# Kernel tuning notes

Measured on AMD Instinct MI355X. Metric: run time of the kernel, lower is better.

The kernel has to match this reference:

```python
import jax, jax.numpy as jnp
import numpy as np

BETA = 0.25


def setup_inputs() -> dict:
    key = jax.random.key(0)
    k1, k2, k3 = jax.random.split(key, 3)
    B, T, D, K = 4, 2048, 512, 16384
    z_e = jax.random.normal(k1, (B, T, D), dtype=jnp.float32)
    codebook = jax.random.normal(k2, (K, D), dtype=jnp.float32)  # frozen embedding
    # nn.Linear(D, D, bias=False) weight, scaled like kaiming-uniform magnitude
    W = jax.random.normal(k3, (D, D), dtype=jnp.float32) * (1.0 / np.sqrt(D))
    return {"z_e": z_e, "codebook": codebook, "W": W}


def reference(z_e, codebook, W):
    B, T, D = z_e.shape
    # effective codebook: Linear(codebook) = codebook @ W.T   -> (K, D)
    eff = jnp.matmul(codebook, W.T)
    z_flat = z_e.reshape(-1, D)  # (N, D)
    # squared euclidean distances (argmin-equivalent to cdist p=2)
    d2 = (
        jnp.sum(z_flat * z_flat, axis=1, keepdims=True)  # (N,1)
        - 2.0 * jnp.matmul(z_flat, eff.T)                  # (N,K)
        + jnp.sum(eff * eff, axis=1)[None, :]              # (1,K)
    )
    code_indices = jnp.argmin(d2, axis=1)  # (N,)
    z_q = eff[code_indices].reshape(B, T, D)
    loss_w = jnp.mean((jax.lax.stop_gradient(z_e) - z_q) ** 2)
    loss_commit = BETA * jnp.mean((z_e - jax.lax.stop_gradient(z_q)) ** 2)
    total_loss = loss_w + loss_commit
    # straight-through estimator
    z_q_out = z_e + jax.lax.stop_gradient(z_q - z_e)
    return z_q_out, total_loss, code_indices.reshape(B, T)
```

## Files before the change

### kernel.cpp

```cpp
#include <hip/hip_runtime.h>
#include <stdint.h>


#define N_ROWS 8192
#define DIM    512
#define K_CB   16384
#define TILE_F16 16384
#define HALF_F16 8192
#define KT_EFF 24
#define KT_D   8
#define TILE_P8 16384
#define HALF_P8 8192
#define PAN_P8  ((size_t)KT_D * TILE_P8)
#define RMARGIN 28.0f

typedef _Float16 f16x8 __attribute__((ext_vector_type(8)));
typedef float f32x4 __attribute__((ext_vector_type(4)));
typedef long lx2 __attribute__((ext_vector_type(2)));

#define FENCE() asm volatile("" ::: "memory")
#define BARRIER() do { FENCE(); __builtin_amdgcn_s_barrier(); FENCE(); } while (0)
#define VMCNT(n) asm volatile("s_waitcnt vmcnt(" #n ")" ::: "memory")

__device__ __forceinline__ void gload_lds16(const void* g, void* l) {
  __builtin_amdgcn_global_load_lds(
      (const __attribute__((address_space(1))) uint32_t*)g,
      (__attribute__((address_space(3))) uint32_t*)l, 16, 0, 0);
}

__device__ __forceinline__ unsigned cvt2_fp8(float a, float b) {
  unsigned r;
  asm("v_cvt_pk_fp8_f32 %0, %1, %2" : "=v"(r) : "v"(a), "v"(b));
  return r & 0xFFFFu;
}

__global__ __launch_bounds__(256) void split_tiled_kernel(
    const float* __restrict__ S, _Float16* __restrict__ T, int resid_limb) {
  const int b = blockIdx.x;
  const int mp = b / 48;
  const int r1 = b % 48;
  const int kt = r1 >> 1, half = r1 & 1;
  const int limb = kt >> 3;
  const int ksrc = (kt & 7) * 64;
  const bool resid = (limb == resid_limb);
  const int t = threadIdx.x;
  _Float16* dst = T + ((size_t)(mp * KT_EFF + kt) * 2 + half) * HALF_F16;
#pragma unroll
  for (int cc = 0; cc < 4; ++cc) {
    const int ci = cc * 256 + t;
    const int kblk = ci >> 7, row = ci & 127;
    const int m = mp * 256 + half * 128 + row;
    const float* src = &S[(size_t)m * DIM + ksrc + kblk * 8];
    float4 x0 = *reinterpret_cast<const float4*>(src);
    float4 x1 = *reinterpret_cast<const float4*>(src + 4);
    const float xs[8] = {x0.x, x0.y, x0.z, x0.w, x1.x, x1.y, x1.z, x1.w};
    f16x8 o;
    if (!resid) {
#pragma unroll
      for (int j = 0; j < 8; ++j) o[j] = (_Float16)xs[j];
    } else {
#pragma unroll
      for (int j = 0; j < 8; ++j) {
        _Float16 h = (_Float16)xs[j];
        o[j] = (_Float16)(xs[j] - (float)h);
      }
    }
    *reinterpret_cast<f16x8*>(&dst[(size_t)ci * 8]) = o;
  }
}

__global__ __launch_bounds__(256) void split1_kernel(
    const float* __restrict__ S, uint8_t* __restrict__ T) {
  const int b = blockIdx.x;
  const int p = b >> 4;
  const int r1 = b & 15;
  const int kt = r1 >> 1, half = r1 & 1;
  const int ksrc = kt * 64;
  const int t = threadIdx.x;
  uint8_t* dst = T + ((size_t)(p * KT_D + kt) * 2 + half) * HALF_P8;
#pragma unroll
  for (int cc = 0; cc < 4; ++cc) {
    const int ci = cc * 256 + t;
    const int kblk = ci >> 7, row = ci & 127;
    const int m = p * 256 + half * 128 + row;
    const float* src = &S[(size_t)m * DIM + ksrc + kblk * 8];
    float4 x0 = *reinterpret_cast<const float4*>(src);
    float4 x1 = *reinterpret_cast<const float4*>(src + 4);
    const unsigned lo = cvt2_fp8(x0.x, x0.y) | (cvt2_fp8(x0.z, x0.w) << 16);
    const unsigned hi = cvt2_fp8(x1.x, x1.y) | (cvt2_fp8(x1.z, x1.w) << 16);
    const uint64_t pack = (uint64_t)lo | ((uint64_t)hi << 32);
    const int q = kblk & 3, h2 = kblk >> 2;
    *reinterpret_cast<uint64_t*>(&dst[(size_t)(q * 128 + row) * 16 + h2 * 8]) =
        pack;
  }
}

__global__ __launch_bounds__(256) void effgemm128_kernel(
    const _Float16* __restrict__ CpT, const _Float16* __restrict__ WpT,
    float* __restrict__ eff, uint8_t* __restrict__ BpT) {
  __shared__ __align__(16) _Float16 lbuf[2][2][HALF_F16];
  const int tid = threadIdx.x;
  const int w = tid >> 6, lane = tid & 63;
  const int lh = lane & 15, lq = lane >> 4;
  const int wr = w >> 1, wc = w & 1;
  const int bid = blockIdx.x;
  const int nb = bid & 3, mh = bid >> 2;
  const int pA = mh >> 1, hA = mh & 1;
  const int pB = nb >> 1, hB = nb & 1;
  f32x4 acc[4][4] = {};

  auto stage = [&](int kt, int buf) {
    const _Float16* a = CpT + (((size_t)pA * KT_EFF + kt) * 2 + hA) * HALF_F16;
    const _Float16* b = WpT + (((size_t)pB * KT_EFF + kt) * 2 + hB) * HALF_F16;
#pragma unroll
    for (int i = 0; i < 4; ++i) {
      const int off = i * 2048 + w * 512;
      gload_lds16(a + off + lane * 8, &lbuf[buf][0][off]);
      gload_lds16(b + off + lane * 8, &lbuf[buf][1][off]);
    }
  };

  stage(0, 0);
  for (int kt = 0; kt < KT_EFF; ++kt) {
    __syncthreads();
    if (kt + 1 < KT_EFF) stage(kt + 1, (kt + 1) & 1);
    const _Float16* At = &lbuf[kt & 1][0][0];
    const _Float16* Bt = &lbuf[kt & 1][1][0];
    f16x8 af[4][2], bf[4][2];
#pragma unroll
    for (int mf = 0; mf < 4; ++mf) {
      const int r = wr * 64 + mf * 16 + lh;
#pragma unroll
      for (int kk = 0; kk < 2; ++kk)
        af[mf][kk] = *reinterpret_cast<const f16x8*>(
            &At[((kk * 4 + lq) * 128 + r) * 8]);
    }
#pragma unroll
    for (int nf = 0; nf < 4; ++nf) {
      const int r = wc * 64 + nf * 16 + lh;
#pragma unroll
      for (int kk = 0; kk < 2; ++kk)
        bf[nf][kk] = *reinterpret_cast<const f16x8*>(
            &Bt[((kk * 4 + lq) * 128 + r) * 8]);
    }
    __builtin_amdgcn_s_setprio(1);
#pragma unroll
    for (int kk = 0; kk < 2; ++kk)
#pragma unroll
      for (int mf = 0; mf < 4; ++mf)
#pragma unroll
        for (int nf = 0; nf < 4; ++nf)
          acc[mf][nf] = __builtin_amdgcn_mfma_f32_16x16x32_f16(
              af[mf][kk], bf[nf][kk], acc[mf][nf], 0, 0, 0);
    __builtin_amdgcn_s_setprio(0);
  }

#pragma unroll
  for (int mf = 0; mf < 4; ++mf)
#pragma unroll
    for (int nf = 0; nf < 4; ++nf) {
      const int cl = wc * 64 + nf * 16 + lh;
      const int col = nb * 128 + cl;
      const int ktd = col >> 6, kd = col & 63;
      const int q = (kd >> 3) & 3, h2 = kd >> 5, jb = kd & 7;
      const unsigned c01 = cvt2_fp8(acc[mf][nf][0], acc[mf][nf][1]);
      const unsigned c23 = cvt2_fp8(acc[mf][nf][2], acc[mf][nf][3]);
#pragma unroll
      for (int j = 0; j < 4; ++j) {
        const int rl = wr * 64 + mf * 16 + lq * 4 + j;
        const int row = mh * 128 + rl;
        eff[(size_t)row * DIM + col] = acc[mf][nf][j];
        const unsigned byte =
            (j < 2 ? (c01 >> (j * 8)) : (c23 >> ((j - 2) * 8))) & 255u;
        BpT[((((size_t)(row >> 8) * KT_D + ktd) * 2 + ((row >> 7) & 1)) * 4 + q)
                * 2048 + (row & 127) * 16 + h2 * 8 + jb] = (uint8_t)byte;
      }
    }
}

__global__ __launch_bounds__(256) void effnorm_kernel(
    const float* __restrict__ E, float* __restrict__ En) {
  const int w = threadIdx.x >> 6;
  const int lane = threadIdx.x & 63;
  const int row = blockIdx.x * 4 + w;
  const float* er = &E[(size_t)row * DIM];
  float s = 0.f;
#pragma unroll
  for (int k = 0; k < DIM / 64; ++k) {
    float v = er[lane + k * 64];
    s = fmaf(v, v, s);
  }
#pragma unroll
  for (int o = 32; o; o >>= 1) s += __shfl_down(s, o, 64);
  if (lane == 0) En[row] = s;
}


__device__ __forceinline__ void stage_half8(const uint8_t* src, uint8_t* ldsb,
                                            int tid) {
  gload_lds16(src + tid * 16, ldsb + tid * 16);
}

template <int MQ>
__device__ __forceinline__ void read_a8(const uint8_t* At, int wr, int lh, int lq,
                                        lx2 af[4]) {
#pragma unroll
  for (int m2 = 0; m2 < 4; ++m2) {
    const int row = wr * 128 + (MQ * 4 + m2) * 16 + lh;
    const int half = row >> 7, r = row & 127;
    af[m2] = *reinterpret_cast<const lx2*>(
        &At[(size_t)half * 8192 + (lq * 128 + r) * 16]);
  }
}

template <int NQ>
__device__ __forceinline__ void read_b8(const uint8_t* Bt, int wc, int lh, int lq,
                                        lx2 bf[4]) {
#pragma unroll
  for (int n2 = 0; n2 < 2; ++n2) {
    const int row = wc * 64 + (NQ * 2 + n2) * 16 + lh;
    const int half = row >> 7, r = row & 127;
    bf[NQ * 2 + n2] = *reinterpret_cast<const lx2*>(
        &Bt[(size_t)half * 8192 + (lq * 128 + r) * 16]);
  }
}

template <int MQ, int NQ>
__device__ __forceinline__ void mfma_phase8(const lx2 af[4], const lx2 bf[4],
                                            f32x4 acc[8][4]) {
  __builtin_amdgcn_s_setprio(1);
#pragma unroll
  for (int kk = 0; kk < 2; ++kk)
#pragma unroll
    for (int m2 = 0; m2 < 4; ++m2)
#pragma unroll
      for (int n2 = 0; n2 < 2; ++n2)
        acc[MQ * 4 + m2][NQ * 2 + n2] = __builtin_amdgcn_mfma_f32_16x16x32_fp8_fp8(
            af[m2][kk], bf[NQ * 2 + n2][kk], acc[MQ * 4 + m2][NQ * 2 + n2], 0, 0, 0);
  __builtin_amdgcn_s_setprio(0);
}

__device__ __forceinline__ void pipeline8_p8(
    const uint8_t* Ab, const uint8_t* Bb, uint8_t (&lds)[4][TILE_P8],
    f32x4 (&acc)[8][4], int tid, int wr, int wc, int lh, int lq, int NT) {
  lx2 af[4], bf[4];
  stage_half8(Ab, &lds[0][0], tid);
  stage_half8(Ab + HALF_P8, &lds[0][HALF_P8], tid);
  stage_half8(Bb, &lds[1][0], tid);
  stage_half8(Bb + HALF_P8, &lds[1][HALF_P8], tid);
  stage_half8(Bb + TILE_P8, &lds[3][0], tid);
  stage_half8(Bb + TILE_P8 + HALF_P8, &lds[3][HALF_P8], tid);
  stage_half8(Ab + TILE_P8, &lds[2][0], tid);
  VMCNT(3);
  BARRIER();
  for (int t = 0; t < NT; ++t) {
    const int s = t & 1;
    const uint8_t* At = &lds[s * 2 + 0][0];
    const uint8_t* Bt = &lds[s * 2 + 1][0];
    read_a8<0>(At, wr, lh, lq, af);
    read_b8<0>(Bt, wc, lh, lq, bf);
    if (t + 1 < NT)
      stage_half8(Ab + (size_t)(t + 1) * TILE_P8 + HALF_P8,
                  &lds[(s ^ 1) * 2][HALF_P8], tid);
    BARRIER();
    mfma_phase8<0, 0>(af, bf, acc);
    BARRIER();
    read_b8<1>(Bt, wc, lh, lq, bf);
    BARRIER();
    mfma_phase8<0, 1>(af, bf, acc);
    BARRIER();
    read_a8<1>(At, wr, lh, lq, af);
    if (t + 2 < NT)
      stage_half8(Bb + (size_t)(t + 2) * TILE_P8, &lds[s * 2 + 1][0], tid);
    BARRIER();
    mfma_phase8<1, 1>(af, bf, acc);
    BARRIER();
    if (t + 2 < NT) {
      stage_half8(Bb + (size_t)(t + 2) * TILE_P8 + HALF_P8,
                  &lds[s * 2 + 1][HALF_P8], tid);
      stage_half8(Ab + (size_t)(t + 2) * TILE_P8, &lds[s * 2][0], tid);
    }
    BARRIER();
    mfma_phase8<1, 0>(af, bf, acc);
    if (t == NT - 2) { VMCNT(0); } else { VMCNT(3); }
    BARRIER();
  }
}

__global__ __launch_bounds__(512) void dist1_kernel(
    const uint8_t* __restrict__ ApT, const uint8_t* __restrict__ BpT,
    const float* __restrict__ En, float* __restrict__ gv,
    unsigned* __restrict__ gmask) {
  __shared__ __align__(16) uint8_t lds[4][TILE_P8];
  const int tid = threadIdx.x;
  const int w = tid >> 6, lane = tid & 63;
  const int lh = lane & 15, lq = lane >> 4;
  const int wr = w >> 2, wc = w & 3;
  const int bid = blockIdx.x;
  const int xcd = bid & 7, c = bid >> 3;
  const int np = xcd * 8 + (c & 7);
  const int mp = c >> 3;
  f32x4 acc[8][4] = {};
  pipeline8_p8(ApT + (size_t)mp * PAN_P8, BpT + (size_t)np * PAN_P8, lds, acc,
               tid, wr, wc, lh, lq, KT_D);
  float en[4];
#pragma unroll
  for (int nf = 0; nf < 4; ++nf)
    en[nf] = En[np * 256 + wc * 64 + nf * 16 + lh];
#pragma unroll
  for (int mf = 0; mf < 8; ++mf) {
#pragma unroll
    for (int j = 0; j < 4; ++j) {
      const float s0 = fmaf(-2.f, acc[mf][0][j], en[0]);
      const float s1 = fmaf(-2.f, acc[mf][1][j], en[1]);
      const float s2 = fmaf(-2.f, acc[mf][2][j], en[2]);
      const float s3 = fmaf(-2.f, acc[mf][3][j], en[3]);
      float v0 = fminf(s0, s1);
      float v1 = fminf(s2, s3);
#pragma unroll
      for (int m = 1; m < 16; m <<= 1) {
        v0 = fminf(v0, __shfl_xor(v0, m, 64));
        v1 = fminf(v1, __shfl_xor(v1, m, 64));
      }
      const unsigned long long b0 = __ballot(s0 <= v0 + RMARGIN);
      const unsigned long long b1 = __ballot(s1 <= v0 + RMARGIN);
      const unsigned long long b2 = __ballot(s2 <= v1 + RMARGIN);
      const unsigned long long b3 = __ballot(s3 <= v1 + RMARGIN);
      if (lh == 0) {
        const int row = mp * 256 + wr * 128 + mf * 16 + lq * 4 + j;
        const unsigned w0 = (unsigned)((b0 >> (lq * 16)) & 0xFFFFull) |
                            ((unsigned)((b1 >> (lq * 16)) & 0xFFFFull) << 16);
        const unsigned w1 = (unsigned)((b2 >> (lq * 16)) & 0xFFFFull) |
                            ((unsigned)((b3 >> (lq * 16)) & 0xFFFFull) << 16);
        float2* gp = (float2*)&gv[(size_t)row * 512 + np * 8 + wc * 2];
        *gp = make_float2(v0, v1);
        uint2* mq = (uint2*)&gmask[(size_t)row * 512 + np * 8 + wc * 2];
        *mq = make_uint2(w0, w1);
      }
    }
  }
}

__global__ __launch_bounds__(256) void refine_kernel(
    const float* __restrict__ Z, const float* __restrict__ E,
    const float* __restrict__ En, const float* __restrict__ gv,
    const unsigned* __restrict__ gmask, float* __restrict__ zq,
    float* __restrict__ out_idx, float* __restrict__ ploss) {
  const int row = blockIdx.x * 4 + (threadIdx.x >> 6);
  const int lane = threadIdx.x & 63;
  const int hl = lane & 31;
  const int hi = lane >> 5;

  float v[8];
#pragma unroll
  for (int i = 0; i < 8; ++i) v[i] = gv[(size_t)row * 512 + i * 64 + lane];
  float A = fminf(fminf(fminf(v[0], v[1]), fminf(v[2], v[3])),
                  fminf(fminf(v[4], v[5]), fminf(v[6], v[7])));
#pragma unroll
  for (int m = 1; m < 64; m <<= 1) A = fminf(A, __shfl_xor(A, m, 64));
  const float thr = A + RMARGIN;

  float4 zr0, zr1, zr2, zr3;
  {
    const float4* zp = (const float4*)(Z + (size_t)row * 512 + hl * 16);
    zr0 = zp[0]; zr1 = zp[1]; zr2 = zp[2]; zr3 = zp[3];
  }

  float bv = 3.0e38f;
  int bi = 2147483647;
#pragma unroll 1
  for (int i = 0; i < 8; ++i) {
    unsigned long long bm = __ballot(v[i] <= thr);
    while (bm) {
      const int l = __builtin_ctzll(bm);
      bm &= bm - 1;
      const int g = i * 64 + l;
      unsigned m = gmask[(size_t)row * 512 + g];
      while (m) {
        const int c0 = __builtin_ctz(m);
        m &= m - 1;
        int c1 = -1;
        if (m) { c1 = __builtin_ctz(m); m &= m - 1; }
        const int cl = hi ? c1 : c0;
        const bool act = (cl >= 0);
        const int col = g * 32 + (act ? cl : c0);
        const float4* er = (const float4*)(E + (size_t)col * 512 + hl * 16);
        const float4 e0 = er[0], e1 = er[1], e2 = er[2], e3 = er[3];
        float p = 0.f;
        p = fmaf(zr0.x, e0.x, p); p = fmaf(zr0.y, e0.y, p);
        p = fmaf(zr0.z, e0.z, p); p = fmaf(zr0.w, e0.w, p);
        p = fmaf(zr1.x, e1.x, p); p = fmaf(zr1.y, e1.y, p);
        p = fmaf(zr1.z, e1.z, p); p = fmaf(zr1.w, e1.w, p);
        p = fmaf(zr2.x, e2.x, p); p = fmaf(zr2.y, e2.y, p);
        p = fmaf(zr2.z, e2.z, p); p = fmaf(zr2.w, e2.w, p);
        p = fmaf(zr3.x, e3.x, p); p = fmaf(zr3.y, e3.y, p);
        p = fmaf(zr3.z, e3.z, p); p = fmaf(zr3.w, e3.w, p);
#pragma unroll
        for (int s2 = 1; s2 < 32; s2 <<= 1) p += __shfl_xor(p, s2, 64);
        const float vv = fmaf(-2.f, p, En[col]);
        if (act && (vv < bv || (vv == bv && col < bi))) { bv = vv; bi = col; }
      }
    }
  }
#pragma unroll
  for (int s2 = 1; s2 < 64; s2 <<= 1) {
    const float v2 = __shfl_xor(bv, s2, 64);
    const int i2 = __shfl_xor(bi, s2, 64);
    if (v2 < bv || (v2 == bv && i2 < bi)) { bv = v2; bi = i2; }
  }
  const int idx = bi;

  const float4* e4 = (const float4*)(E + (size_t)idx * 512 + lane * 8);
  const float4* z4 = (const float4*)(Z + (size_t)row * 512 + lane * 8);
  float4* q4 = (float4*)(zq + (size_t)row * 512 + lane * 8);
  const float4 ea = e4[0], eb = e4[1];
  const float4 za = z4[0], zb = z4[1];
  q4[0] = ea; q4[1] = eb;
  float s = 0.f;
  s = fmaf(za.x - ea.x, za.x - ea.x, s); s = fmaf(za.y - ea.y, za.y - ea.y, s);
  s = fmaf(za.z - ea.z, za.z - ea.z, s); s = fmaf(za.w - ea.w, za.w - ea.w, s);
  s = fmaf(zb.x - eb.x, zb.x - eb.x, s); s = fmaf(zb.y - eb.y, zb.y - eb.y, s);
  s = fmaf(zb.z - eb.z, zb.z - eb.z, s); s = fmaf(zb.w - eb.w, zb.w - eb.w, s);
#pragma unroll
  for (int o = 32; o; o >>= 1) s += __shfl_down(s, o, 64);
  if (lane == 0) {
    ploss[row] = s;
    out_idx[row] = (float)idx;
  }
}

__global__ __launch_bounds__(256) void loss_final_kernel(
    const float* __restrict__ ploss, float* __restrict__ out_loss) {
  const int t = threadIdx.x;
  double s = 0.0;
  for (int i = t; i < N_ROWS; i += 256) s += (double)ploss[i];
#pragma unroll
  for (int o = 32; o; o >>= 1) s += __shfl_down(s, o, 64);
  __shared__ double ds[4];
  if ((t & 63) == 0) ds[t >> 6] = s;
  __syncthreads();
  if (t == 0) {
    double tot = ds[0] + ds[1] + ds[2] + ds[3];
    out_loss[0] = (float)(1.25 * tot / ((double)N_ROWS * (double)DIM));
  }
}


extern "C" void kernel_launch(void* const* d_in, const int* in_sizes, int n_in,
                              void* d_out, int out_size, void* d_ws, size_t ws_size,
                              hipStream_t stream) {
  const float* z_e      = (const float*)d_in[0];
  const float* codebook = (const float*)d_in[1];
  const float* W        = (const float*)d_in[2];
  float* out = (float*)d_out;
  char* ws = (char*)d_ws;

  float*          eff     = (float*)(ws);
  float*          effnorm = (float*)(ws + 33554432);
  _Float16*       WpT     = (_Float16*)(ws + 33619968);
  float*          ploss   = (float*)(ws + 36274176);
  _Float16*       CpT     = (_Float16*)(ws + 36306944);
  float*          gv      = (float*)(ws + 36306944);
  uint8_t*        ApT     = (uint8_t*)(ws + 53084160);
  unsigned*       gmask   = (unsigned*)(ws + 61472768);
  uint8_t*        BpT     = (uint8_t*)(ws + 86638592);

  float* out_zq   = out;
  float* out_loss = out + (size_t)N_ROWS * DIM;
  float* out_idx  = out + (size_t)N_ROWS * DIM + 1;

  split_tiled_kernel<<<64 * 48, 256, 0, stream>>>(codebook, CpT, 2);
  split_tiled_kernel<<<2 * 48, 256, 0, stream>>>(W, WpT, 1);
  effgemm128_kernel<<<512, 256, 0, stream>>>(CpT, WpT, eff, BpT);
  effnorm_kernel<<<K_CB / 4, 256, 0, stream>>>(eff, effnorm);
  split1_kernel<<<32 * 16, 256, 0, stream>>>(z_e, ApT);
  dist1_kernel<<<2048, 512, 0, stream>>>(ApT, BpT, effnorm, gv, gmask);
  refine_kernel<<<N_ROWS / 4, 256, 0, stream>>>(z_e, eff, effnorm, gv, gmask,
                                                out_zq, out_idx, ploss);
  loss_final_kernel<<<1, 256, 0, stream>>>(ploss, out_loss);
}
```

Baseline: 295.6 us.

## Add fp16 intermediate screening stage in refine before exact fp32 rescoring

Adds a kernel that converts the effective codebook to fp16. The refine kernel now scores the fp8-screened candidates with fp16 codebook rows, which halves the gather bytes per candidate, and stores the scores in shared memory. Only candidates within a small margin of the fp16 minimum are then rescored exactly in fp32 over the full wavefront. This cuts fp32 gather traffic in refine, at the cost of an extra conversion pass over the 32 MB codebook, a third screening stage, and a risk of mis-selection if the fp16 error exceeds the 0.5 margin.

Result: slower. 302.8 us (+2.4%).

```diff
diff --git a/kernel.cpp b/kernel.cpp
--- a/kernel.cpp
+++ b/kernel.cpp
@@ -13,6 +13,8 @@
 #define HALF_P8 8192
 #define PAN_P8  ((size_t)KT_D * TILE_P8)
 #define RMARGIN 28.0f
+#define TMARG   0.5f
+#define MAXC    256
 
 typedef _Float16 f16x8 __attribute__((ext_vector_type(8)));
 typedef float f32x4 __attribute__((ext_vector_type(4)));
@@ -176,6 +178,24 @@
                 * 2048 + (row & 127) * 16 + h2 * 8 + jb] = (uint8_t)byte;
       }
     }
+}
+
+__global__ __launch_bounds__(256) void eff16_kernel(
+    const float* __restrict__ E, _Float16* __restrict__ E16) {
+  const size_t base = ((size_t)blockIdx.x * 256 + threadIdx.x) * 16;
+  const float4* s = (const float4*)(E + base);
+  const float4 a = s[0], b = s[1], c = s[2], d = s[3];
+  f16x8 lo, hi;
+  lo[0] = (_Float16)a.x; lo[1] = (_Float16)a.y;
+  lo[2] = (_Float16)a.z; lo[3] = (_Float16)a.w;
+  lo[4] = (_Float16)b.x; lo[5] = (_Float16)b.y;
+  lo[6] = (_Float16)b.z; lo[7] = (_Float16)b.w;
+  hi[0] = (_Float16)c.x; hi[1] = (_Float16)c.y;
+  hi[2] = (_Float16)c.z; hi[3] = (_Float16)c.w;
+  hi[4] = (_Float16)d.x; hi[5] = (_Float16)d.y;
+  hi[6] = (_Float16)d.z; hi[7] = (_Float16)d.w;
+  *reinterpret_cast<f16x8*>(E16 + base) = lo;
+  *reinterpret_cast<f16x8*>(E16 + base + 8) = hi;
 }
 
 __global__ __launch_bounds__(256) void effnorm_kernel(
@@ -343,13 +363,17 @@
 
 __global__ __launch_bounds__(256) void refine_kernel(
     const float* __restrict__ Z, const float* __restrict__ E,
-    const float* __restrict__ En, const float* __restrict__ gv,
-    const unsigned* __restrict__ gmask, float* __restrict__ zq,
-    float* __restrict__ out_idx, float* __restrict__ ploss) {
-  const int row = blockIdx.x * 4 + (threadIdx.x >> 6);
+    const _Float16* __restrict__ E16, const float* __restrict__ En,
+    const float* __restrict__ gv, const unsigned* __restrict__ gmask,
+    float* __restrict__ zq, float* __restrict__ out_idx,
+    float* __restrict__ ploss) {
+  const int w = threadIdx.x >> 6;
+  const int row = blockIdx.x * 4 + w;
   const int lane = threadIdx.x & 63;
   const int hl = lane & 31;
   const int hi = lane >> 5;
+  __shared__ float ss[4][MAXC];
+  __shared__ int sc[4][MAXC];
 
   float v[8];
 #pragma unroll
@@ -365,9 +389,27 @@
     const float4* zp = (const float4*)(Z + (size_t)row * 512 + hl * 16);
     zr0 = zp[0]; zr1 = zp[1]; zr2 = zp[2]; zr3 = zp[3];
   }
+  const float4* z4 = (const float4*)(Z + (size_t)row * 512 + lane * 8);
+  const float4 za = z4[0], zb = z4[1];
 
   float bv = 3.0e38f;
   int bi = 2147483647;
+
+  auto exact64 = [&](int colu) {
+    const float4* er = (const float4*)(E + (size_t)colu * 512 + lane * 8);
+    const float4 ea4 = er[0], eb4 = er[1];
+    float p = 0.f;
+    p = fmaf(za.x, ea4.x, p); p = fmaf(za.y, ea4.y, p);
+    p = fmaf(za.z, ea4.z, p); p = fmaf(za.w, ea4.w, p);
+    p = fmaf(zb.x, eb4.x, p); p = fmaf(zb.y, eb4.y, p);
+    p = fmaf(zb.z, eb4.z, p); p = fmaf(zb.w, eb4.w, p);
+#pragma unroll
+    for (int s2 = 1; s2 < 64; s2 <<= 1) p += __shfl_xor(p, s2, 64);
+    const float vv = fmaf(-2.f, p, En[colu]);
+    if (vv < bv || (vv == bv && colu < bi)) { bv = vv; bi = colu; }
+  };
+
+  int nc = 0;
 #pragma unroll 1
   for (int i = 0; i < 8; ++i) {
     unsigned long long bm = __ballot(v[i] <= thr);
@@ -381,40 +423,53 @@
         m &= m - 1;
         int c1 = -1;
         if (m) { c1 = __builtin_ctz(m); m &= m - 1; }
+        const bool act = (c1 >= 0);
         const int cl = hi ? c1 : c0;
-        const bool act = (cl >= 0);
-        const int col = g * 32 + (act ? cl : c0);
-        const float4* er = (const float4*)(E + (size_t)col * 512 + hl * 16);
-        const float4 e0 = er[0], e1 = er[1], e2 = er[2], e3 = er[3];
-        float p = 0.f;
-        p = fmaf(zr0.x, e0.x, p); p = fmaf(zr0.y, e0.y, p);
-        p = fmaf(zr0.z, e0.z, p); p = fmaf(zr0.w, e0.w, p);
-        p = fmaf(zr1.x, e1.x, p); p = fmaf(zr1.y, e1.y, p);
-        p = fmaf(zr1.z, e1.z, p); p = fmaf(zr1.w, e1.w, p);
-        p = fmaf(zr2.x, e2.x, p); p = fmaf(zr2.y, e2.y, p);
-        p = fmaf(zr2.z, e2.z, p); p = fmaf(zr2.w, e2.w, p);
-        p = fmaf(zr3.x, e3.x, p); p = fmaf(zr3.y, e3.y, p);
-        p = fmaf(zr3.z, e3.z, p); p = fmaf(zr3.w, e3.w, p);
-#pragma unroll
-        for (int s2 = 1; s2 < 32; s2 <<= 1) p += __shfl_xor(p, s2, 64);
-        const float vv = fmaf(-2.f, p, En[col]);
-        if (act && (vv < bv || (vv == bv && col < bi))) { bv = vv; bi = col; }
+        const int col = g * 32 + ((hi && act) ? c1 : c0);
+        (void)cl;
+        if (nc < MAXC - 1) {
+          const f16x8 ea = *reinterpret_cast<const f16x8*>(
+              E16 + (size_t)col * 512 + hl * 16);
+          const f16x8 eb = *reinterpret_cast<const f16x8*>(
+              E16 + (size_t)col * 512 + hl * 16 + 8);
+          float p = 0.f;
+          p = fmaf((float)ea[0], zr0.x, p); p = fmaf((float)ea[1], zr0.y, p);
+          p = fmaf((float)ea[2], zr0.z, p); p = fmaf((float)ea[3], zr0.w, p);
+          p = fmaf((float)ea[4], zr1.x, p); p = fmaf((float)ea[5], zr1.y, p);
+          p = fmaf((float)ea[6], zr1.z, p); p = fmaf((float)ea[7], zr1.w, p);
+          p = fmaf((float)eb[0], zr2.x, p); p = fmaf((float)eb[1], zr2.y, p);
+          p = fmaf((float)eb[2], zr2.z, p); p = fmaf((float)eb[3], zr2.w, p);
+          p = fmaf((float)eb[4], zr3.x, p); p = fmaf((float)eb[5], zr3.y, p);
+          p = fmaf((float)eb[6], zr3.z, p); p = fmaf((float)eb[7], zr3.w, p);
+#pragma unroll
+          for (int s2 = 1; s2 < 32; s2 <<= 1) p += __shfl_xor(p, s2, 64);
+          const float vv = fmaf(-2.f, p, En[col]);
+          if (lane == 0) { ss[w][nc] = vv; sc[w][nc] = col; }
+          if (lane == 32 && act) { ss[w][nc + 1] = vv; sc[w][nc + 1] = col; }
+          nc += act ? 2 : 1;
+        } else {
+          exact64(g * 32 + c0);
+          if (act) exact64(g * 32 + c1);
+        }
       }
     }
   }
-#pragma unroll
-  for (int s2 = 1; s2 < 64; s2 <<= 1) {
-    const float v2 = __shfl_xor(bv, s2, 64);
-    const int i2 = __shfl_xor(bi, s2, 64);
-    if (v2 < bv || (v2 == bv && i2 < bi)) { bv = v2; bi = i2; }
+
+  float m16 = 3.0e38f;
+  for (int q = lane; q < nc; q += 64) m16 = fminf(m16, ss[w][q]);
+#pragma unroll
+  for (int s2 = 1; s2 < 64; s2 <<= 1) m16 = fminf(m16, __shfl_xor(m16, s2, 64));
+  const float thr2 = m16 + TMARG;
+#pragma unroll 1
+  for (int q = 0; q < nc; ++q) {
+    const float sv = ss[w][q];
+    if (sv <= thr2) exact64(sc[w][q]);
   }
   const int idx = bi;
 
   const float4* e4 = (const float4*)(E + (size_t)idx * 512 + lane * 8);
-  const float4* z4 = (const float4*)(Z + (size_t)row * 512 + lane * 8);
   float4* q4 = (float4*)(zq + (size_t)row * 512 + lane * 8);
   const float4 ea = e4[0], eb = e4[1];
-  const float4 za = z4[0], zb = z4[1];
   q4[0] = ea; q4[1] = eb;
   float s = 0.f;
   s = fmaf(za.x - ea.x, za.x - ea.x, s); s = fmaf(za.y - ea.y, za.y - ea.y, s);
@@ -461,9 +516,10 @@
   float*          ploss   = (float*)(ws + 36274176);
   _Float16*       CpT     = (_Float16*)(ws + 36306944);
   float*          gv      = (float*)(ws + 36306944);
-  uint8_t*        ApT     = (uint8_t*)(ws + 53084160);
-  unsigned*       gmask   = (unsigned*)(ws + 61472768);
+  unsigned*       gmask   = (unsigned*)(ws + 53084160);
+  _Float16*       eff16   = (_Float16*)(ws + 69861376);
   uint8_t*        BpT     = (uint8_t*)(ws + 86638592);
+  uint8_t*        ApT     = (uint8_t*)(ws + 95027200);
 
   float* out_zq   = out;
   float* out_loss = out + (size_t)N_ROWS * DIM;
@@ -472,10 +528,11 @@
   split_tiled_kernel<<<64 * 48, 256, 0, stream>>>(codebook, CpT, 2);
   split_tiled_kernel<<<2 * 48, 256, 0, stream>>>(W, WpT, 1);
   effgemm128_kernel<<<512, 256, 0, stream>>>(CpT, WpT, eff, BpT);
+  eff16_kernel<<<2048, 256, 0, stream>>>(eff, eff16);
   effnorm_kernel<<<K_CB / 4, 256, 0, stream>>>(eff, effnorm);
   split1_kernel<<<32 * 16, 256, 0, stream>>>(z_e, ApT);
   dist1_kernel<<<2048, 512, 0, stream>>>(ApT, BpT, effnorm, gv, gmask);
-  refine_kernel<<<N_ROWS / 4, 256, 0, stream>>>(z_e, eff, effnorm, gv, gmask,
-                                                out_zq, out_idx, ploss);
+  refine_kernel<<<N_ROWS / 4, 256, 0, stream>>>(z_e, eff, eff16, effnorm, gv,
+                                                gmask, out_zq, out_idx, ploss);
   loss_final_kernel<<<1, 256, 0, stream>>>(ploss, out_loss);
 }
```
